# Optimization experiments

Hardware: AMD Instinct MI355X
Metric: run time of the kernel (lower is better)

The kernel has to match this reference:

```python
import jax, jax.numpy as jnp
import numpy as np

T, B, INP, HID = 256, 128, 512, 512
LAST_K, RSIZE = 32, 64
ATTN = 1.0
NEG = -1e30  # stands in for float('-inf') in the mask; softmax weight is exactly 0 either way


def setup_inputs() -> dict:
    key = jax.random.key(0)
    ks = jax.random.split(key, 6)
    xav = lambda fi, fo: (2.0 / (fi + fo)) ** 0.5
    x = jax.random.normal(ks[0], (T, B, INP), jnp.float32)
    # torch Linear weights stored transposed so y = x @ W (+ b)
    Uw = jax.random.normal(ks[1], (INP, HID), jnp.float32) * xav(INP, HID)
    Ub = jnp.zeros((HID,), jnp.float32)
    Vw = jax.random.normal(ks[2], (HID, HID), jnp.float32) * xav(HID, HID)
    Uaw = jax.random.normal(ks[3], (HID, HID), jnp.float32) * xav(HID, HID)
    Vaw = jax.random.normal(ks[4], (HID, HID), jnp.float32) * xav(HID, HID)
    v = jax.random.normal(ks[5], (HID,), jnp.float32) * xav(1, HID)
    return {"x": x, "Uw": Uw, "Ub": Ub, "Vw": Vw, "Uaw": Uaw, "Vaw": Vaw, "v": v}


def reference(x, Uw, Ub, Vw, Uaw, Vaw, v):
    Tlen, Bsz, _ = x.shape
    H = Uw.shape[1]
    bidx = jnp.arange(Bsz)

    def step(carry, inp):
        xt, t = inp
        st, buf, slot_time, long_mem, long_mask, long_scores, buck, fcnt, lids = carry

        def first(_):
            # hidden is None -> zeros, so V(hidden) == 0; st is the pre-nonlinearity h
            pre = xt @ Uw + Ub
            return pre, jnp.tanh(pre), long_scores

        def later(_):
            va_st = st @ Vaw                                  # [B,H]
            # short-term memory attention (buf slot p holds h_{slot_time[p]}, -1 = empty)
            es = jnp.einsum('kbh,h->kb', jnp.tanh(va_st[None] + buf @ Uaw), v)
            es = jnp.where(slot_time[:, None] >= 0, es, NEG)  # mask empty slots
            es_l = jnp.einsum('rbh,h->rb', jnp.tanh(va_st[None] + long_mem @ Uaw), v) + long_mask
            alphas = jax.nn.softmax(jnp.concatenate([es, es_l], axis=0), axis=0)  # [K+R,B]
            comb = jnp.concatenate([buf, long_mem], axis=0)   # [K+R,B,H]
            ct = jnp.einsum('mb,mbh->bh', alphas, comb)
            last_h = buf[(t - 1) % LAST_K]                    # memory[-1] == h_{t-1}
            st_new = 0.5 * (last_h + ct * ATTN)
            h = jnp.tanh(xt @ Uw + Ub + st_new @ Vw)
            # detached accumulation of attention mass per timestep (long_scores[time] += alpha)
            det = jax.lax.stop_gradient(alphas[:LAST_K])
            valid = slot_time >= 0
            ls = long_scores.at[jnp.where(valid, slot_time, 0)].add(
                jnp.where(valid[:, None], det, 0.0))
            return st_new, h, ls

        st, h, long_scores = jax.lax.cond(t == 0, first, later, None)

        # --- conditional bucket eviction: candidate is h_{t-LAST_K} (oldest in buf) ---
        evict_step = t >= LAST_K
        cand = buf[t % LAST_K]                                # slot about to be overwritten
        score_t = long_scores[jnp.maximum(t - LAST_K, 0)]     # [B]
        minp = jnp.argmin(buck, axis=1)                       # [B]
        not_full = fcnt < RSIZE
        replace = score_t > buck[bidx, minp]
        do = evict_step & (not_full | replace)
        pos = jnp.where(not_full, fcnt, minp)                 # [B]
        long_mem = long_mem.at[pos, bidx].set(jnp.where(do[:, None], cand, long_mem[pos, bidx]))
        long_mask = long_mask.at[pos, bidx].set(jnp.where(do, 0.0, long_mask[pos, bidx]))
        buck = buck.at[bidx, pos].set(jnp.where(do, score_t, buck[bidx, pos]))
        lids = lids.at[bidx, pos].set(jnp.where(do, (t - LAST_K).astype(jnp.float32), lids[bidx, pos]))
        fcnt = jnp.where(do & not_full, fcnt + 1, fcnt)

        # append h to short-term circular buffer
        buf = buf.at[t % LAST_K].set(h)
        slot_time = slot_time.at[t % LAST_K].set(t)

        return (st, buf, slot_time, long_mem, long_mask, long_scores, buck, fcnt, lids), h

    carry0 = (
        jnp.zeros((Bsz, H), jnp.float32),                 # st
        jnp.zeros((LAST_K, Bsz, H), jnp.float32),         # short-term memory buffer
        -jnp.ones((LAST_K,), jnp.int32),                  # time stored in each buf slot
        jnp.zeros((RSIZE, Bsz, H), jnp.float32),          # long_mem buckets
        jnp.full((RSIZE, Bsz), NEG, jnp.float32),         # long_mask
        jnp.zeros((Tlen, Bsz), jnp.float32),              # long_scores
        jnp.zeros((Bsz, RSIZE), jnp.float32),             # buck_scores
        jnp.zeros((Bsz,), jnp.int32),                     # bucket fill count
        -jnp.ones((Bsz, RSIZE), jnp.float32),             # long_ids
    )
    _, hs = jax.lax.scan(step, carry0, (x, jnp.arange(Tlen)))
    return hs  # [T,B,H] hidden state at every step
```

## Files before the change

### kernel.cpp

```cpp
#include <hip/hip_runtime.h>
#include <hip/hip_bf16.h>
#include <cstddef>

#define kT 256
#define kB 128
#define kINP 512
#define kH 512
#define kK 32
#define kR 64
#define kNEG (-1e30f)

__device__ __forceinline__ void ag_store(float* p, float v) {
    __hip_atomic_store(p, v, __ATOMIC_RELAXED, __HIP_MEMORY_SCOPE_AGENT);
}
__device__ __forceinline__ float ag_load(const float* p) {
    return __hip_atomic_load(p, __ATOMIC_RELAXED, __HIP_MEMORY_SCOPE_AGENT);
}

__device__ __forceinline__ float ftanh(float x)
{
    float e = __expf(2.0f * x);
    return 1.0f - 2.0f * __builtin_amdgcn_rcpf(e + 1.0f);
}

__global__ __launch_bounds__(256) void gemm_xu(
    const float* __restrict__ A, const float* __restrict__ W,
    const float* __restrict__ bias, float* __restrict__ C,
    int M, int N, int K)
{
    __shared__ float As[32][36];
    __shared__ float Ws[32][68];
    const int tid = threadIdx.x;
    const int n0 = blockIdx.x * 64;
    const int m0 = blockIdx.y * 32;
    const int ty = tid >> 4, tx = tid & 15;
    const int arow = tid >> 3, ac4 = (tid & 7) << 2;
    const int wrow = tid >> 4, wc4 = (tid & 15) << 2;

    float acc[2][4] = {};

    for (int k0 = 0; k0 < K; k0 += 32) {
        float4 av = *reinterpret_cast<const float4*>(&A[(size_t)(m0 + arow) * K + k0 + ac4]);
        float4 w0 = *reinterpret_cast<const float4*>(&W[(size_t)(k0 + wrow) * N + n0 + wc4]);
        float4 w1 = *reinterpret_cast<const float4*>(&W[(size_t)(k0 + wrow + 16) * N + n0 + wc4]);
        *reinterpret_cast<float4*>(&As[arow][ac4]) = av;
        *reinterpret_cast<float4*>(&Ws[wrow][wc4]) = w0;
        *reinterpret_cast<float4*>(&Ws[wrow + 16][wc4]) = w1;
        __syncthreads();
#pragma unroll
        for (int kk = 0; kk < 32; ++kk) {
            float a0 = As[ty * 2 + 0][kk];
            float a1 = As[ty * 2 + 1][kk];
            float4 wv = *reinterpret_cast<float4*>(&Ws[kk][tx * 4]);
            acc[0][0] += a0 * wv.x; acc[0][1] += a0 * wv.y;
            acc[0][2] += a0 * wv.z; acc[0][3] += a0 * wv.w;
            acc[1][0] += a1 * wv.x; acc[1][1] += a1 * wv.y;
            acc[1][2] += a1 * wv.z; acc[1][3] += a1 * wv.w;
        }
        __syncthreads();
    }

#pragma unroll
    for (int r = 0; r < 2; ++r) {
        int m = m0 + ty * 2 + r;
#pragma unroll
        for (int j = 0; j < 4; ++j) {
            int n = n0 + tx * 4 + j;
            C[(size_t)m * N + n] = acc[r][j] + bias[n];
        }
    }
}

__global__ __launch_bounds__(256) void init_flags_k(int* __restrict__ flags)
{
    int i = blockIdx.x * 256 + threadIdx.x;
    if (i < kB * 3 * 2) flags[i] = 0;
}

__global__ __launch_bounds__(1024) void rnn_pair(
    const float* __restrict__ Vw, const float* __restrict__ Vaw,
    const float* __restrict__ Uaw, const float* __restrict__ vvec,
    const float* __restrict__ XU, float* __restrict__ lngU,
    float* __restrict__ hs, float* __restrict__ esx,
    float* __restrict__ stx, int* __restrict__ flags)
{
    extern __shared__ float dyn[];
    float* shortH = dyn;
    float* shortU = dyn + 32 * 256;
    float* longH  = dyn + 64 * 256;
    float* part   = dyn + 128 * 256;
    const int PSTR = 264;

    const int bid = blockIdx.x;
    const int b = bid >> 1, half = bid & 1;
    const int C0 = half << 8;
    const int P0 = (half ^ 1) << 8;
    const int tid = threadIdx.x;
    const int kq = tid >> 6;
    const int lane = tid & 63;
    const int c4 = lane << 2;

    __shared__ __align__(16) float h_sh[512];
    __shared__ __align__(16) float st_sh[512];
    __shared__ __align__(16) float va_sh[256];
    __shared__ __align__(16) float v_sh[256];
    __shared__ float es_own[96], es_sh[96], w_sh[96];
    __shared__ int   rowm[96];
    __shared__ float lsc_sh[kT];
    __shared__ float buck_sh[kR];
    __shared__ int   lidx_sh[kR];
    __shared__ int   fcnt_sh, evict_pos;
    __shared__ float red0, red1;

    float* lngU_b = lngU + (size_t)bid * kR * 256;

    int* fC_own = &flags[(b * 3 + 0) * 2 + half];
    int* fB_own = &flags[(b * 3 + 1) * 2 + half];
    int* fS_own = &flags[(b * 3 + 2) * 2 + half];
    int* fC_par = &flags[(b * 3 + 0) * 2 + (half ^ 1)];
    int* fB_par = &flags[(b * 3 + 1) * 2 + (half ^ 1)];
    int* fS_par = &flags[(b * 3 + 2) * 2 + (half ^ 1)];

    auto wait_ge = [&](int* f, int target) {
        if (tid == 0) {
            while (__hip_atomic_load(f, __ATOMIC_RELAXED, __HIP_MEMORY_SCOPE_AGENT) < target)
                __builtin_amdgcn_s_sleep(1);
        }
        __syncthreads();
    };
    auto set_flag = [&](int* f, int val) {
        __syncthreads();
        if (tid == 0)
            __hip_atomic_store(f, val, __ATOMIC_RELAXED, __HIP_MEMORY_SCOPE_AGENT);
    };

    if (tid < 256) { v_sh[tid] = vvec[C0 + tid]; lsc_sh[tid] = 0.0f; }
    if (tid < kR) { buck_sh[tid] = 0.0f; lidx_sh[tid] = -1; }
    if (tid == 0) fcnt_sh = 0;
    if (tid < 512) st_sh[tid] = XU[(size_t)b * kH + tid];
    __syncthreads();
    if (tid < 256) {
        float h0 = tanhf(st_sh[C0 + tid]);
        h_sh[C0 + tid] = h0;
        shortH[tid] = h0;
        ag_store(&hs[(size_t)b * kH + C0 + tid], h0);
    }
    set_flag(fC_own, 1);
    {
        float4 acc = {0, 0, 0, 0};
#pragma unroll 8
        for (int k = kq; k < kH; k += 16) {
            float s = st_sh[k];
            const float4 w = *reinterpret_cast<const float4*>(&Vaw[(size_t)k * kH + C0 + c4]);
            acc.x += s * w.x; acc.y += s * w.y; acc.z += s * w.z; acc.w += s * w.w;
        }
        *reinterpret_cast<float4*>(&part[kq * PSTR + c4]) = acc;
        __syncthreads();
        if (tid < 256) {
            float s = 0.0f;
#pragma unroll
            for (int j = 0; j < 16; ++j) s += part[j * PSTR + tid];
            va_sh[tid] = s;
        }
        __syncthreads();
    }

    for (int t = 1; t < kT; ++t) {
        float xu_reg = 0.0f;
        if (tid < 256) xu_reg = XU[((size_t)t * kB + b) * kH + C0 + tid];

        float4 accA = {0, 0, 0, 0};
#pragma unroll 8
        for (int k = C0 + kq; k < C0 + 256; k += 16) {
            float s = h_sh[k];
            const float4 w = *reinterpret_cast<const float4*>(&Uaw[(size_t)k * kH + C0 + c4]);
            accA.x += s * w.x; accA.y += s * w.y; accA.z += s * w.z; accA.w += s * w.w;
        }
        if (tid < 96) {
            int row;
            if (tid < kK) { int md = (t + 31 - tid) & 31; row = t - 1 - md; }
            else row = lidx_sh[tid - kK];
            rowm[tid] = row;
        }
        wait_ge(fC_par, t);
        if (tid < 256) h_sh[P0 + tid] = ag_load(&hs[((size_t)(t - 1) * kB + b) * kH + P0 + tid]);
        __syncthreads();
#pragma unroll 8
        for (int k = P0 + kq; k < P0 + 256; k += 16) {
            float s = h_sh[k];
            const float4 w = *reinterpret_cast<const float4*>(&Uaw[(size_t)k * kH + C0 + c4]);
            accA.x += s * w.x; accA.y += s * w.y; accA.z += s * w.z; accA.w += s * w.w;
        }
        *reinterpret_cast<float4*>(&part[kq * PSTR + c4]) = accA;
        __syncthreads();
        if (tid < 256) {
            float u = 0.0f;
#pragma unroll
            for (int j = 0; j < 16; ++j) u += part[j * PSTR + tid];
            shortU[((t - 1) & 31) * 256 + tid] = u;
        }
        __syncthreads();

        {
            float4 uu[6];
            int rv[6];
#pragma unroll
            for (int r = 0; r < 6; ++r) {
                int m = kq + (r << 4);
                int row = rowm[m];
                rv[r] = row;
                uu[r] = make_float4(0.f, 0.f, 0.f, 0.f);
                if (row >= 0) {
                    const float* up = (m < kK) ? &shortU[m * 256]
                                               : &lngU_b[(size_t)(m - kK) * 256];
                    uu[r] = *reinterpret_cast<const float4*>(&up[c4]);
                }
            }
            const float4 vav = *reinterpret_cast<const float4*>(&va_sh[c4]);
            const float4 vvv = *reinterpret_cast<const float4*>(&v_sh[c4]);
#pragma unroll
            for (int r = 0; r < 6; ++r) {
                float p = 0.0f;
                if (rv[r] >= 0) {
                    p = vvv.x * ftanh(vav.x + uu[r].x) + vvv.y * ftanh(vav.y + uu[r].y)
                      + vvv.z * ftanh(vav.z + uu[r].z) + vvv.w * ftanh(vav.w + uu[r].w);
                }
#pragma unroll
                for (int off = 32; off; off >>= 1) p += __shfl_down(p, off);
                if (lane == 0) es_own[kq + (r << 4)] = p;
            }
        }
        __syncthreads();
        if (tid < 96) ag_store(&esx[((size_t)b * 2 + half) * 96 + tid], es_own[tid]);
        set_flag(fB_own, t);
        wait_ge(fB_par, t);
        if (tid < 96) {
            float e = kNEG;
            if (rowm[tid] >= 0)
                e = es_own[tid] + ag_load(&esx[((size_t)b * 2 + (half ^ 1)) * 96 + tid]);
            es_sh[tid] = e;
        }
        __syncthreads();

        if (tid < 64) {
            float a = es_sh[tid];
            float c = (tid < 32) ? es_sh[64 + tid] : kNEG;
            float mx = fmaxf(a, c);
#pragma unroll
            for (int off = 32; off; off >>= 1) mx = fmaxf(mx, __shfl_xor(mx, off));
            if (tid == 0) red0 = mx;
        }
        __syncthreads();
        if (tid < 96) w_sh[tid] = __expf(es_sh[tid] - red0);
        __syncthreads();
        if (tid < 64) {
            float a = w_sh[tid] + ((tid < 32) ? w_sh[64 + tid] : 0.0f);
#pragma unroll
            for (int off = 32; off; off >>= 1) a += __shfl_xor(a, off);
            if (tid == 0) red1 = 1.0f / a;
        }
        __syncthreads();

        {
            float4 acc = {0, 0, 0, 0};
#pragma unroll
            for (int r = 0; r < 6; ++r) {
                int m = kq + (r << 4);
                int row = rowm[m];
                if (row >= 0) {
                    const float* hp = (m < kK) ? &shortH[m * 256]
                                               : &longH[(m - kK) * 256];
                    const float4 hv = *reinterpret_cast<const float4*>(&hp[c4]);
                    float wgt = w_sh[m];
                    acc.x += wgt * hv.x; acc.y += wgt * hv.y;
                    acc.z += wgt * hv.z; acc.w += wgt * hv.w;
                }
            }
            *reinterpret_cast<float4*>(&part[kq * PSTR + c4]) = acc;
        }
        __syncthreads();
        if (tid < 256) {
            float ct = 0.0f;
#pragma unroll
            for (int j = 0; j < 16; ++j) ct += part[j * PSTR + tid];
            float stv = 0.5f * (h_sh[C0 + tid] + ct * red1);
            st_sh[C0 + tid] = stv;
            ag_store(&stx[(size_t)b * kH + C0 + tid], stv);
        }
        set_flag(fS_own, t);

        if (tid < kK) {
            int row = rowm[tid];
            if (row >= 0) lsc_sh[row] += w_sh[tid] * red1;
        }
        __syncthreads();
        if (tid == 0) {
            int ep = -1;
            if (t >= kK) {
                float score = lsc_sh[t - kK];
                int fc = fcnt_sh;
                bool nf = fc < kR;
                float mn = buck_sh[0]; int mp = 0;
                for (int r = 1; r < kR; ++r) {
                    float bv = buck_sh[r];
                    if (bv < mn) { mn = bv; mp = r; }
                }
                if (nf || score > mn) {
                    ep = nf ? fc : mp;
                    lidx_sh[ep] = t - kK;
                    buck_sh[ep] = score;
                    if (nf) fcnt_sh = fc + 1;
                }
            }
            evict_pos = ep;
        }
        __syncthreads();
        if (evict_pos >= 0 && tid < 256) {
            longH[evict_pos * 256 + tid] = shortH[(t & 31) * 256 + tid];
            lngU_b[(size_t)evict_pos * 256 + tid] = shortU[(t & 31) * 256 + tid];
        }

        {
            float4 aw = {0, 0, 0, 0};
#pragma unroll 8
            for (int k = C0 + kq; k < C0 + 256; k += 16) {
                float s = st_sh[k];
                const float4 w = *reinterpret_cast<const float4*>(&Vw[(size_t)k * kH + C0 + c4]);
                aw.x += s * w.x; aw.y += s * w.y; aw.z += s * w.z; aw.w += s * w.w;
            }
            wait_ge(fS_par, t);
            if (tid < 256) st_sh[P0 + tid] = ag_load(&stx[(size_t)b * kH + P0 + tid]);
            __syncthreads();
#pragma unroll 8
            for (int k = P0 + kq; k < P0 + 256; k += 16) {
                float s = st_sh[k];
                const float4 w = *reinterpret_cast<const float4*>(&Vw[(size_t)k * kH + C0 + c4]);
                aw.x += s * w.x; aw.y += s * w.y; aw.z += s * w.z; aw.w += s * w.w;
            }
            *reinterpret_cast<float4*>(&part[kq * PSTR + c4]) = aw;
        }
        __syncthreads();
        if (tid < 256) {
            float hpre = xu_reg;
#pragma unroll
            for (int j = 0; j < 16; ++j) hpre += part[j * PSTR + tid];
            float hv = tanhf(hpre);
            h_sh[C0 + tid] = hv;
            shortH[(t & 31) * 256 + tid] = hv;
            ag_store(&hs[((size_t)t * kB + b) * kH + C0 + tid], hv);
        }
        set_flag(fC_own, t + 1);

        {
            float4 av = {0, 0, 0, 0};
#pragma unroll 8
            for (int k = kq; k < kH; k += 16) {
                float s = st_sh[k];
                const float4 w = *reinterpret_cast<const float4*>(&Vaw[(size_t)k * kH + C0 + c4]);
                av.x += s * w.x; av.y += s * w.y; av.z += s * w.z; av.w += s * w.w;
            }
            *reinterpret_cast<float4*>(&part[kq * PSTR + c4]) = av;
        }
        __syncthreads();
        if (tid < 256) {
            float vn = 0.0f;
#pragma unroll
            for (int j = 0; j < 16; ++j) vn += part[j * PSTR + tid];
            va_sh[tid] = vn;
        }
        __syncthreads();
    }
}

extern "C" void kernel_launch(void* const* d_in, const int* in_sizes, int n_in,
                              void* d_out, int out_size, void* d_ws, size_t ws_size,
                              hipStream_t stream)
{
    const float* x   = (const float*)d_in[0];
    const float* Uw  = (const float*)d_in[1];
    const float* Ub  = (const float*)d_in[2];
    const float* Vw  = (const float*)d_in[3];
    const float* Uaw = (const float*)d_in[4];
    const float* Vaw = (const float*)d_in[5];
    const float* vv  = (const float*)d_in[6];
    float* hs = (float*)d_out;

    float* ws = (float*)d_ws;
    const size_t TBH = (size_t)kT * kB * kH;
    float* XU   = ws;
    float* lngU = XU + TBH;
    float* esx  = lngU + (size_t)2 * kB * kR * 256;
    float* stx  = esx + (size_t)kB * 2 * 96;
    int*   flags = (int*)(stx + (size_t)kB * kH);

    const int dyn_bytes = (32 * 256 + 32 * 256 + 64 * 256 + 16 * 264) * 4;
    static int lds_cfg = 0;
    if (!lds_cfg) {
        hipFuncSetAttribute(reinterpret_cast<const void*>(rnn_pair),
                            hipFuncAttributeMaxDynamicSharedMemorySize, dyn_bytes);
        lds_cfg = 1;
    }

    init_flags_k<<<3, 256, 0, stream>>>(flags);

    gemm_xu<<<dim3(kH / 64, (kT * kB) / 32), 256, 0, stream>>>(
        x, Uw, Ub, XU, kT * kB, kH, kINP);

    rnn_pair<<<2 * kB, 1024, dyn_bytes, stream>>>(
        Vw, Vaw, Uaw, vv, XU, lngU, hs, esx, stx, flags);
}
```

Before: 5.630 ms.

## Restructure RNN step: fuse Vaw matvec with Uaw pass, trim barriers, retile XU GEMM

The GEMM for x@U is retiled to 64x64 blocks with a 4x4 per-thread micro-tile and a transposed A tile in LDS. In the recurrent kernel, the st@Vaw matvec moves from the end of each step into the start of the next, where it shares a reduction barrier with the Uaw pass. Softmax max and sum are now computed redundantly per wave with shuffles instead of block reductions through shared scalars, which removes several __syncthreads per step. Flag waits spin on every thread instead of one thread plus a barrier. Long-term H memory moves from LDS to global workspace to shrink LDS, which adds global loads in the context sum.

```diff
diff --git a/kernel.cpp b/kernel.cpp
--- a/kernel.cpp
+++ b/kernel.cpp
@@ -25,48 +25,53 @@
 
 __global__ __launch_bounds__(256) void gemm_xu(
     const float* __restrict__ A, const float* __restrict__ W,
-    const float* __restrict__ bias, float* __restrict__ C,
-    int M, int N, int K)
-{
-    __shared__ float As[32][36];
+    const float* __restrict__ bias, float* __restrict__ C)
+{
+    __shared__ float At[32][68];
     __shared__ float Ws[32][68];
     const int tid = threadIdx.x;
     const int n0 = blockIdx.x * 64;
-    const int m0 = blockIdx.y * 32;
-    const int ty = tid >> 4, tx = tid & 15;
-    const int arow = tid >> 3, ac4 = (tid & 7) << 2;
-    const int wrow = tid >> 4, wc4 = (tid & 15) << 2;
-
-    float acc[2][4] = {};
-
-    for (int k0 = 0; k0 < K; k0 += 32) {
-        float4 av = *reinterpret_cast<const float4*>(&A[(size_t)(m0 + arow) * K + k0 + ac4]);
-        float4 w0 = *reinterpret_cast<const float4*>(&W[(size_t)(k0 + wrow) * N + n0 + wc4]);
-        float4 w1 = *reinterpret_cast<const float4*>(&W[(size_t)(k0 + wrow + 16) * N + n0 + wc4]);
-        *reinterpret_cast<float4*>(&As[arow][ac4]) = av;
-        *reinterpret_cast<float4*>(&Ws[wrow][wc4]) = w0;
-        *reinterpret_cast<float4*>(&Ws[wrow + 16][wc4]) = w1;
+    const int m0 = blockIdx.y * 64;
+    const int tx = tid & 15, ty = tid >> 4;
+    const int arow = tid >> 3, ak = (tid & 7) << 2;
+    const int wrow = tid >> 4, wc = (tid & 15) << 2;
+
+    float acc[4][4] = {};
+
+    for (int k0 = 0; k0 < kINP; k0 += 32) {
+        float4 a0 = *reinterpret_cast<const float4*>(&A[(size_t)(m0 + arow) * kINP + k0 + ak]);
+        float4 a1 = *reinterpret_cast<const float4*>(&A[(size_t)(m0 + 32 + arow) * kINP + k0 + ak]);
+        float4 w0 = *reinterpret_cast<const float4*>(&W[(size_t)(k0 + wrow) * kH + n0 + wc]);
+        float4 w1 = *reinterpret_cast<const float4*>(&W[(size_t)(k0 + wrow + 16) * kH + n0 + wc]);
+        __syncthreads();
+        At[ak + 0][arow] = a0.x; At[ak + 1][arow] = a0.y;
+        At[ak + 2][arow] = a0.z; At[ak + 3][arow] = a0.w;
+        At[ak + 0][32 + arow] = a1.x; At[ak + 1][32 + arow] = a1.y;
+        At[ak + 2][32 + arow] = a1.z; At[ak + 3][32 + arow] = a1.w;
+        *reinterpret_cast<float4*>(&Ws[wrow][wc]) = w0;
+        *reinterpret_cast<float4*>(&Ws[wrow + 16][wc]) = w1;
         __syncthreads();
 #pragma unroll
         for (int kk = 0; kk < 32; ++kk) {
-            float a0 = As[ty * 2 + 0][kk];
-            float a1 = As[ty * 2 + 1][kk];
-            float4 wv = *reinterpret_cast<float4*>(&Ws[kk][tx * 4]);
-            acc[0][0] += a0 * wv.x; acc[0][1] += a0 * wv.y;
-            acc[0][2] += a0 * wv.z; acc[0][3] += a0 * wv.w;
-            acc[1][0] += a1 * wv.x; acc[1][1] += a1 * wv.y;
-            acc[1][2] += a1 * wv.z; acc[1][3] += a1 * wv.w;
-        }
-        __syncthreads();
+            float4 a4 = *reinterpret_cast<float4*>(&At[kk][ty * 4]);
+            float4 w4 = *reinterpret_cast<float4*>(&Ws[kk][tx * 4]);
+            float a_[4] = {a4.x, a4.y, a4.z, a4.w};
+            float w_[4] = {w4.x, w4.y, w4.z, w4.w};
+#pragma unroll
+            for (int r = 0; r < 4; ++r)
+#pragma unroll
+                for (int c = 0; c < 4; ++c)
+                    acc[r][c] += a_[r] * w_[c];
+        }
     }
 
 #pragma unroll
-    for (int r = 0; r < 2; ++r) {
-        int m = m0 + ty * 2 + r;
-#pragma unroll
-        for (int j = 0; j < 4; ++j) {
-            int n = n0 + tx * 4 + j;
-            C[(size_t)m * N + n] = acc[r][j] + bias[n];
+    for (int r = 0; r < 4; ++r) {
+        int m = m0 + ty * 4 + r;
+#pragma unroll
+        for (int c = 0; c < 4; ++c) {
+            int n = n0 + tx * 4 + c;
+            C[(size_t)m * kH + n] = acc[r][c] + bias[n];
         }
     }
 }
@@ -81,15 +86,15 @@
     const float* __restrict__ Vw, const float* __restrict__ Vaw,
     const float* __restrict__ Uaw, const float* __restrict__ vvec,
     const float* __restrict__ XU, float* __restrict__ lngU,
-    float* __restrict__ hs, float* __restrict__ esx,
-    float* __restrict__ stx, int* __restrict__ flags)
+    float* __restrict__ lngH, float* __restrict__ hs,
+    float* __restrict__ esx, float* __restrict__ stx, int* __restrict__ flags)
 {
     extern __shared__ float dyn[];
     float* shortH = dyn;
     float* shortU = dyn + 32 * 256;
-    float* longH  = dyn + 64 * 256;
-    float* part   = dyn + 128 * 256;
-    const int PSTR = 264;
+    float* part   = dyn + 64 * 256;
+    float* part2  = part + 16 * 260;
+    const int PSTR = 260;
 
     const int bid = blockIdx.x;
     const int b = bid >> 1, half = bid & 1;
@@ -104,15 +109,15 @@
     __shared__ __align__(16) float st_sh[512];
     __shared__ __align__(16) float va_sh[256];
     __shared__ __align__(16) float v_sh[256];
-    __shared__ float es_own[96], es_sh[96], w_sh[96];
+    __shared__ float es_own[96], es_sh[96];
     __shared__ int   rowm[96];
     __shared__ float lsc_sh[kT];
     __shared__ float buck_sh[kR];
     __shared__ int   lidx_sh[kR];
     __shared__ int   fcnt_sh, evict_pos;
-    __shared__ float red0, red1;
 
     float* lngU_b = lngU + (size_t)bid * kR * 256;
+    float* lngH_b = lngH + (size_t)bid * kR * 256;
 
     int* fC_own = &flags[(b * 3 + 0) * 2 + half];
     int* fB_own = &flags[(b * 3 + 1) * 2 + half];
@@ -121,12 +126,9 @@
     int* fB_par = &flags[(b * 3 + 1) * 2 + (half ^ 1)];
     int* fS_par = &flags[(b * 3 + 2) * 2 + (half ^ 1)];
 
-    auto wait_ge = [&](int* f, int target) {
-        if (tid == 0) {
-            while (__hip_atomic_load(f, __ATOMIC_RELAXED, __HIP_MEMORY_SCOPE_AGENT) < target)
-                __builtin_amdgcn_s_sleep(1);
-        }
-        __syncthreads();
+    auto spin_ge = [&](int* f, int target) {
+        while (__hip_atomic_load(f, __ATOMIC_RELAXED, __HIP_MEMORY_SCOPE_AGENT) < target)
+            __builtin_amdgcn_s_sleep(2);
     };
     auto set_flag = [&](int* f, int val) {
         __syncthreads();
@@ -146,35 +148,23 @@
         ag_store(&hs[(size_t)b * kH + C0 + tid], h0);
     }
     set_flag(fC_own, 1);
-    {
-        float4 acc = {0, 0, 0, 0};
+
+    for (int t = 1; t < kT; ++t) {
+        float xu_reg = (tid < 256) ? XU[((size_t)t * kB + b) * kH + C0 + tid] : 0.0f;
+
+        float4 av4 = {0, 0, 0, 0};
 #pragma unroll 8
         for (int k = kq; k < kH; k += 16) {
             float s = st_sh[k];
             const float4 w = *reinterpret_cast<const float4*>(&Vaw[(size_t)k * kH + C0 + c4]);
-            acc.x += s * w.x; acc.y += s * w.y; acc.z += s * w.z; acc.w += s * w.w;
-        }
-        *reinterpret_cast<float4*>(&part[kq * PSTR + c4]) = acc;
-        __syncthreads();
-        if (tid < 256) {
-            float s = 0.0f;
-#pragma unroll
-            for (int j = 0; j < 16; ++j) s += part[j * PSTR + tid];
-            va_sh[tid] = s;
-        }
-        __syncthreads();
-    }
-
-    for (int t = 1; t < kT; ++t) {
-        float xu_reg = 0.0f;
-        if (tid < 256) xu_reg = XU[((size_t)t * kB + b) * kH + C0 + tid];
-
-        float4 accA = {0, 0, 0, 0};
+            av4.x += s * w.x; av4.y += s * w.y; av4.z += s * w.z; av4.w += s * w.w;
+        }
+        float4 au4 = {0, 0, 0, 0};
 #pragma unroll 8
         for (int k = C0 + kq; k < C0 + 256; k += 16) {
             float s = h_sh[k];
             const float4 w = *reinterpret_cast<const float4*>(&Uaw[(size_t)k * kH + C0 + c4]);
-            accA.x += s * w.x; accA.y += s * w.y; accA.z += s * w.z; accA.w += s * w.w;
+            au4.x += s * w.x; au4.y += s * w.y; au4.z += s * w.z; au4.w += s * w.w;
         }
         if (tid < 96) {
             int row;
@@ -182,33 +172,35 @@
             else row = lidx_sh[tid - kK];
             rowm[tid] = row;
         }
-        wait_ge(fC_par, t);
+        spin_ge(fC_par, t);
         if (tid < 256) h_sh[P0 + tid] = ag_load(&hs[((size_t)(t - 1) * kB + b) * kH + P0 + tid]);
         __syncthreads();
 #pragma unroll 8
         for (int k = P0 + kq; k < P0 + 256; k += 16) {
             float s = h_sh[k];
             const float4 w = *reinterpret_cast<const float4*>(&Uaw[(size_t)k * kH + C0 + c4]);
-            accA.x += s * w.x; accA.y += s * w.y; accA.z += s * w.z; accA.w += s * w.w;
-        }
-        *reinterpret_cast<float4*>(&part[kq * PSTR + c4]) = accA;
+            au4.x += s * w.x; au4.y += s * w.y; au4.z += s * w.z; au4.w += s * w.w;
+        }
+        *reinterpret_cast<float4*>(&part[kq * PSTR + c4]) = au4;
+        *reinterpret_cast<float4*>(&part2[kq * PSTR + c4]) = av4;
         __syncthreads();
         if (tid < 256) {
-            float u = 0.0f;
-#pragma unroll
-            for (int j = 0; j < 16; ++j) u += part[j * PSTR + tid];
+            float u = 0.0f, va = 0.0f;
+#pragma unroll
+            for (int j = 0; j < 16; ++j) { u += part[j * PSTR + tid]; va += part2[j * PSTR + tid]; }
             shortU[((t - 1) & 31) * 256 + tid] = u;
+            va_sh[tid] = va;
         }
         __syncthreads();
 
         {
-            float4 uu[6];
-            int rv[6];
+            float4 uu[6]; int rv[6];
+            const float4 vav = *reinterpret_cast<const float4*>(&va_sh[c4]);
+            const float4 vvv = *reinterpret_cast<const float4*>(&v_sh[c4]);
 #pragma unroll
             for (int r = 0; r < 6; ++r) {
                 int m = kq + (r << 4);
-                int row = rowm[m];
-                rv[r] = row;
+                int row = rowm[m]; rv[r] = row;
                 uu[r] = make_float4(0.f, 0.f, 0.f, 0.f);
                 if (row >= 0) {
                     const float* up = (m < kK) ? &shortU[m * 256]
@@ -216,8 +208,6 @@
                     uu[r] = *reinterpret_cast<const float4*>(&up[c4]);
                 }
             }
-            const float4 vav = *reinterpret_cast<const float4*>(&va_sh[c4]);
-            const float4 vvv = *reinterpret_cast<const float4*>(&v_sh[c4]);
 #pragma unroll
             for (int r = 0; r < 6; ++r) {
                 float p = 0.0f;
@@ -227,13 +217,15 @@
                 }
 #pragma unroll
                 for (int off = 32; off; off >>= 1) p += __shfl_down(p, off);
-                if (lane == 0) es_own[kq + (r << 4)] = p;
-            }
-        }
-        __syncthreads();
-        if (tid < 96) ag_store(&esx[((size_t)b * 2 + half) * 96 + tid], es_own[tid]);
+                if (lane == 0) {
+                    int m = kq + (r << 4);
+                    es_own[m] = p;
+                    ag_store(&esx[((size_t)b * 2 + half) * 96 + m], p);
+                }
+            }
+        }
         set_flag(fB_own, t);
-        wait_ge(fB_par, t);
+        spin_ge(fB_par, t);
         if (tid < 96) {
             float e = kNEG;
             if (rowm[tid] >= 0)
@@ -242,39 +234,39 @@
         }
         __syncthreads();
 
-        if (tid < 64) {
-            float a = es_sh[tid];
-            float c = (tid < 32) ? es_sh[64 + tid] : kNEG;
-            float mx = fmaxf(a, c);
-#pragma unroll
-            for (int off = 32; off; off >>= 1) mx = fmaxf(mx, __shfl_xor(mx, off));
-            if (tid == 0) red0 = mx;
-        }
-        __syncthreads();
-        if (tid < 96) w_sh[tid] = __expf(es_sh[tid] - red0);
-        __syncthreads();
-        if (tid < 64) {
-            float a = w_sh[tid] + ((tid < 32) ? w_sh[64 + tid] : 0.0f);
-#pragma unroll
-            for (int off = 32; off; off >>= 1) a += __shfl_xor(a, off);
-            if (tid == 0) red1 = 1.0f / a;
-        }
-        __syncthreads();
-
+        float mx, inv;
         {
-            float4 acc = {0, 0, 0, 0};
+            float a = es_sh[lane];
+            float b2 = (lane < 32) ? es_sh[64 + lane] : kNEG;
+            float m2 = fmaxf(a, b2);
+#pragma unroll
+            for (int off = 32; off; off >>= 1) m2 = fmaxf(m2, __shfl_xor(m2, off));
+            mx = m2;
+            float e = __expf(a - mx) + ((lane < 32) ? __expf(b2 - mx) : 0.0f);
+#pragma unroll
+            for (int off = 32; off; off >>= 1) e += __shfl_xor(e, off);
+            inv = 1.0f / e;
+        }
+
+        {
+            float4 hv[6]; float wq[6];
 #pragma unroll
             for (int r = 0; r < 6; ++r) {
                 int m = kq + (r << 4);
                 int row = rowm[m];
+                hv[r] = make_float4(0.f, 0.f, 0.f, 0.f); wq[r] = 0.0f;
                 if (row >= 0) {
                     const float* hp = (m < kK) ? &shortH[m * 256]
-                                               : &longH[(m - kK) * 256];
-                    const float4 hv = *reinterpret_cast<const float4*>(&hp[c4]);
-                    float wgt = w_sh[m];
-                    acc.x += wgt * hv.x; acc.y += wgt * hv.y;
-                    acc.z += wgt * hv.z; acc.w += wgt * hv.w;
-                }
+                                               : &lngH_b[(size_t)(m - kK) * 256];
+                    hv[r] = *reinterpret_cast<const float4*>(&hp[c4]);
+                    wq[r] = __expf(es_sh[m] - mx);
+                }
+            }
+            float4 acc = {0, 0, 0, 0};
+#pragma unroll
+            for (int r = 0; r < 6; ++r) {
+                acc.x += wq[r] * hv[r].x; acc.y += wq[r] * hv[r].y;
+                acc.z += wq[r] * hv[r].z; acc.w += wq[r] * hv[r].w;
             }
             *reinterpret_cast<float4*>(&part[kq * PSTR + c4]) = acc;
         }
@@ -283,7 +275,7 @@
             float ct = 0.0f;
 #pragma unroll
             for (int j = 0; j < 16; ++j) ct += part[j * PSTR + tid];
-            float stv = 0.5f * (h_sh[C0 + tid] + ct * red1);
+            float stv = 0.5f * (h_sh[C0 + tid] + ct * inv);
             st_sh[C0 + tid] = stv;
             ag_store(&stx[(size_t)b * kH + C0 + tid], stv);
         }
@@ -291,9 +283,8 @@
 
         if (tid < kK) {
             int row = rowm[tid];
-            if (row >= 0) lsc_sh[row] += w_sh[tid] * red1;
-        }
-        __syncthreads();
+            if (row >= 0) lsc_sh[row] += __expf(es_sh[tid] - mx) * inv;
+        }
         if (tid == 0) {
             int ep = -1;
             if (t >= kK) {
@@ -316,59 +307,38 @@
         }
         __syncthreads();
         if (evict_pos >= 0 && tid < 256) {
-            longH[evict_pos * 256 + tid] = shortH[(t & 31) * 256 + tid];
+            lngH_b[(size_t)evict_pos * 256 + tid] = shortH[(t & 31) * 256 + tid];
             lngU_b[(size_t)evict_pos * 256 + tid] = shortU[(t & 31) * 256 + tid];
         }
 
-        {
-            float4 aw = {0, 0, 0, 0};
-#pragma unroll 8
-            for (int k = C0 + kq; k < C0 + 256; k += 16) {
-                float s = st_sh[k];
-                const float4 w = *reinterpret_cast<const float4*>(&Vw[(size_t)k * kH + C0 + c4]);
-                aw.x += s * w.x; aw.y += s * w.y; aw.z += s * w.z; aw.w += s * w.w;
-            }
-            wait_ge(fS_par, t);
-            if (tid < 256) st_sh[P0 + tid] = ag_load(&stx[(size_t)b * kH + P0 + tid]);
-            __syncthreads();
-#pragma unroll 8
-            for (int k = P0 + kq; k < P0 + 256; k += 16) {
-                float s = st_sh[k];
-                const float4 w = *reinterpret_cast<const float4*>(&Vw[(size_t)k * kH + C0 + c4]);
-                aw.x += s * w.x; aw.y += s * w.y; aw.z += s * w.z; aw.w += s * w.w;
-            }
-            *reinterpret_cast<float4*>(&part[kq * PSTR + c4]) = aw;
-        }
+        float4 aw4 = {0, 0, 0, 0};
+#pragma unroll 8
+        for (int k = C0 + kq; k < C0 + 256; k += 16) {
+            float s = st_sh[k];
+            const float4 w = *reinterpret_cast<const float4*>(&Vw[(size_t)k * kH + C0 + c4]);
+            aw4.x += s * w.x; aw4.y += s * w.y; aw4.z += s * w.z; aw4.w += s * w.w;
+        }
+        spin_ge(fS_par, t);
+        if (tid < 256) st_sh[P0 + tid] = ag_load(&stx[(size_t)b * kH + P0 + tid]);
+        __syncthreads();
+#pragma unroll 8
+        for (int k = P0 + kq; k < P0 + 256; k += 16) {
+            float s = st_sh[k];
+            const float4 w = *reinterpret_cast<const float4*>(&Vw[(size_t)k * kH + C0 + c4]);
+            aw4.x += s * w.x; aw4.y += s * w.y; aw4.z += s * w.z; aw4.w += s * w.w;
+        }
+        *reinterpret_cast<float4*>(&part[kq * PSTR + c4]) = aw4;
         __syncthreads();
         if (tid < 256) {
             float hpre = xu_reg;
 #pragma unroll
             for (int j = 0; j < 16; ++j) hpre += part[j * PSTR + tid];
-            float hv = tanhf(hpre);
-            h_sh[C0 + tid] = hv;
-            shortH[(t & 31) * 256 + tid] = hv;
-            ag_store(&hs[((size_t)t * kB + b) * kH + C0 + tid], hv);
+            float hval = tanhf(hpre);
+            h_sh[C0 + tid] = hval;
+            shortH[(t & 31) * 256 + tid] = hval;
+            ag_store(&hs[((size_t)t * kB + b) * kH + C0 + tid], hval);
         }
         set_flag(fC_own, t + 1);
-
-        {
-            float4 av = {0, 0, 0, 0};
-#pragma unroll 8
-            for (int k = kq; k < kH; k += 16) {
-                float s = st_sh[k];
-                const float4 w = *reinterpret_cast<const float4*>(&Vaw[(size_t)k * kH + C0 + c4]);
-                av.x += s * w.x; av.y += s * w.y; av.z += s * w.z; av.w += s * w.w;
-            }
-            *reinterpret_cast<float4*>(&part[kq * PSTR + c4]) = av;
-        }
-        __syncthreads();
-        if (tid < 256) {
-            float vn = 0.0f;
-#pragma unroll
-            for (int j = 0; j < 16; ++j) vn += part[j * PSTR + tid];
-            va_sh[tid] = vn;
-        }
-        __syncthreads();
     }
 }
 
@@ -389,23 +359,19 @@
     const size_t TBH = (size_t)kT * kB * kH;
     float* XU   = ws;
     float* lngU = XU + TBH;
-    float* esx  = lngU + (size_t)2 * kB * kR * 256;
+    float* lngH = lngU + (size_t)2 * kB * kR * 256;
+    float* esx  = lngH + (size_t)2 * kB * kR * 256;
     float* stx  = esx + (size_t)kB * 2 * 96;
     int*   flags = (int*)(stx + (size_t)kB * kH);
 
-    const int dyn_bytes = (32 * 256 + 32 * 256 + 64 * 256 + 16 * 264) * 4;
-    static int lds_cfg = 0;
-    if (!lds_cfg) {
-        hipFuncSetAttribute(reinterpret_cast<const void*>(rnn_pair),
-                            hipFuncAttributeMaxDynamicSharedMemorySize, dyn_bytes);
-        lds_cfg = 1;
-    }
+    const int dyn_bytes = (64 * 256 + 2 * 16 * 260) * 4;
+    hipFuncSetAttribute(reinterpret_cast<const void*>(rnn_pair),
+                        hipFuncAttributeMaxDynamicSharedMemorySize, dyn_bytes);
 
     init_flags_k<<<3, 256, 0, stream>>>(flags);
 
-    gemm_xu<<<dim3(kH / 64, (kT * kB) / 32), 256, 0, stream>>>(
-        x, Uw, Ub, XU, kT * kB, kH, kINP);
+    gemm_xu<<<dim3(kH / 64, (kT * kB) / 64), 256, 0, stream>>>(x, Uw, Ub, XU);
 
     rnn_pair<<<2 * kB, 1024, dyn_bytes, stream>>>(
-        Vw, Vaw, Uaw, vv, XU, lngU, hs, esx, stx, flags);
-}
+        Vw, Vaw, Uaw, vv, XU, lngU, lngH, hs, esx, stx, flags);
+}
```

Result: slower. 11.51 ms (+104.4%).
